# Performance work log

Hardware: AMD Instinct MI355X
Metric: run time of the kernel (lower is better)

The kernel has to match this reference:

```python
import jax, jax.numpy as jnp
import numpy as np

N_HEAD = 12


def setup_inputs() -> dict:
    key = jax.random.key(0)
    ks = jax.random.split(key, 6)
    B, T, C = 8, 1024, 768
    x = jax.random.normal(ks[0], (B, T, C), dtype=jnp.float32)
    w_attn = jax.random.normal(ks[1], (C, 3 * C), dtype=jnp.float32) * 0.02
    b_attn = jnp.zeros((3 * C,), dtype=jnp.float32)
    w_proj = jax.random.normal(ks[2], (C, C), dtype=jnp.float32) * 0.02
    b_proj = jnp.zeros((C,), dtype=jnp.float32)
    rel_emb = jax.random.normal(ks[3], (2 * 1024 - 1, C // N_HEAD), dtype=jnp.float32) * 0.02
    return {"x": x, "w_attn": w_attn, "b_attn": b_attn,
            "w_proj": w_proj, "b_proj": b_proj, "rel_emb": rel_emb}


def reference(x, w_attn, b_attn, w_proj, b_proj, rel_emb):
    b, t, c = x.shape
    h = N_HEAD
    d = c // h
    scale = d ** -0.5
    # fused QKV projection
    qkv = x @ w_attn + b_attn                       # [b, t, 3c]
    q, k, v = jnp.split(qkv, 3, axis=-1)
    split_heads = lambda z: z.reshape(b, t, h, d).transpose(0, 2, 1, 3)  # [b,h,t,d]
    q, k, v = map(split_heads, (q, k, v))
    q = q * scale
    # content scores
    scores = jnp.einsum('bhid,bhjd->bhij', q, k)    # [b,h,t,t]
    # relative position bias: embed lookup + rel-shift (zero row prepended, last dropped)
    rel = rel_emb[:t]                               # [t, d]
    rel = jnp.concatenate([jnp.zeros_like(rel[:1]), rel], axis=0)[:-1]
    scores = scores + jnp.einsum('bhid,jd->bhij', q, rel)
    # causal mask
    causal = jnp.tril(jnp.ones((t, t), dtype=bool))
    scores = jnp.where(causal, scores, -jnp.inf)
    probs = jax.nn.softmax(scores, axis=-1)
    y = jnp.einsum('bhij,bhjd->bhid', probs, v)     # [b,h,t,d]
    y = y.transpose(0, 2, 1, 3).reshape(b, t, c)
    return y @ w_proj + b_proj
```

## Files before the change

### kernel.cpp

```cpp
#include <hip/hip_runtime.h>
#include <stdint.h>


typedef __attribute__((ext_vector_type(8))) short short8;
typedef __attribute__((ext_vector_type(4))) float f32x4;
typedef __attribute__((ext_vector_type(4))) unsigned short ushort4v;

#define DEV static __device__ __forceinline__

DEV float bf2f(unsigned short u) {
    union { unsigned int u; float f; } v; v.u = ((unsigned int)u) << 16; return v.f;
}
DEV unsigned short f2bf(float f) {
    union { float f; unsigned int u; } v; v.f = f;
    unsigned int u = v.u;
    return (unsigned short)((u + 0x7fffu + ((u >> 16) & 1u)) >> 16);
}

typedef const __attribute__((address_space(1))) void* gas_ptr;
typedef __attribute__((address_space(3))) void* las_ptr;
DEV void glds16(const void* g, void* l) {
    __builtin_amdgcn_global_load_lds((gas_ptr)g, (las_ptr)l, 16, 0, 0);
}

__global__ void detect_dtype(const unsigned int* __restrict__ w, int* __restrict__ flag) {
    __shared__ int cnt;
    if (threadIdx.x == 0) cnt = 0;
    __syncthreads();
    int c = 0;
    for (int i = threadIdx.x; i < 8192; i += 256) {
        unsigned int b1 = (w[i] >> 8) & 0x7F;
        c += (b1 >= 0x38 && b1 <= 0x3E) ? 1 : 0;
    }
    atomicAdd(&cnt, c);
    __syncthreads();
    if (threadIdx.x == 0) *flag = (cnt > 4096) ? 1 : 0;
}

__global__ __launch_bounds__(256) void cast_x(
    const void* __restrict__ x, unsigned short* __restrict__ xo,
    const int* __restrict__ flag)
{
    int i = (blockIdx.x * 256 + threadIdx.x) * 4;
    if (*flag) {
        *(ushort4v*)(xo + i) = *(const ushort4v*)((const unsigned short*)x + i);
    } else {
        f32x4 v = *(const f32x4*)((const float*)x + i);
        ushort4v o;
#pragma unroll
        for (int j = 0; j < 4; ++j) o[j] = f2bf(v[j]);
        *(ushort4v*)(xo + i) = o;
    }
}

__global__ __launch_bounds__(256) void cast_small(
    const void* __restrict__ rel, const void* __restrict__ ba, const void* __restrict__ bp,
    unsigned short* __restrict__ rel_o, unsigned short* __restrict__ ba_o,
    unsigned short* __restrict__ bp_o, const int* __restrict__ flag)
{
    int i = blockIdx.x * 256 + threadIdx.x;
    if (i >= 134080) return;
    int isbf = *flag;
    const void* src; unsigned short* dst; int off;
    if (i < 131008)      { src = rel; dst = rel_o; off = i; }
    else if (i < 133312) { src = ba;  dst = ba_o;  off = i - 131008; }
    else                 { src = bp;  dst = bp_o;  off = i - 133312; }
    dst[off] = isbf ? ((const unsigned short*)src)[off]
                    : f2bf(((const float*)src)[off]);
}

__global__ __launch_bounds__(256) void transpose_w(
    const void* __restrict__ in, unsigned short* __restrict__ out,
    int R, int C, const int* __restrict__ flag)
{
    __shared__ unsigned short tile[64][66];
    const int t = threadIdx.x;
    const int cb = blockIdx.x * 64;
    const int rb = blockIdx.y * 64;
    if (*flag) {
        const unsigned short* inp = (const unsigned short*)in;
        const int c8 = (t & 7) * 8;
        const int r = t >> 3;
#pragma unroll
        for (int p = 0; p < 2; ++p) {
            int rr = r + p * 32;
            short8 v = *(const short8*)(inp + (size_t)(rb + rr) * C + cb + c8);
#pragma unroll
            for (int i = 0; i < 8; ++i) tile[rr][c8 + i] = (unsigned short)v[i];
        }
    } else {
        const float* inp = (const float*)in;
        const int c4 = (t & 15) * 4;
        const int r = t >> 4;
#pragma unroll
        for (int p = 0; p < 4; ++p) {
            int rr = r + p * 16;
            f32x4 v = *(const f32x4*)(inp + (size_t)(rb + rr) * C + cb + c4);
#pragma unroll
            for (int i = 0; i < 4; ++i) tile[rr][c4 + i] = f2bf(v[i]);
        }
    }
    __syncthreads();
    {
        const int c8 = (t & 7) * 8;
        const int r = t >> 3;
#pragma unroll
        for (int p = 0; p < 2; ++p) {
            int oc = r + p * 32;
            short8 v;
#pragma unroll
            for (int i = 0; i < 8; ++i) v[i] = (short)tile[c8 + i][oc];
            *(short8*)(out + (size_t)(cb + oc) * R + rb + c8) = v;
        }
    }
}

#define GEMM_PROLOG(A_, Bt_)                                                     \
    __shared__ __align__(16) unsigned short Abuf[128 * 32];                      \
    __shared__ __align__(16) unsigned short Bbuf[128 * 32];                      \
    const int t = threadIdx.x;                                                   \
    const int wave = t >> 6, lane = t & 63;                                      \
    const int lo = lane & 15, hi = lane >> 4;                                    \
    const int wr = wave >> 1, wc = wave & 1;                                     \
    const int bm = blockIdx.x * 128;                                             \
    const int bn = blockIdx.y * 128;                                             \
    int L0 = t << 4, L1 = (t + 256) << 4;                                        \
    int S0 = L0 ^ (((L0 >> 7) & 3) << 4);                                        \
    int S1 = L1 ^ (((L1 >> 7) & 3) << 4);                                        \
    int r0 = S0 >> 6, o0 = (S0 & 63) >> 1;                                       \
    int r1 = S1 >> 6, o1 = (S1 & 63) >> 1;                                       \
    const unsigned short* Ab = (A_) + (size_t)bm * 768;                          \
    const unsigned short* Bb = (Bt_) + (size_t)bn * 768;                         \
    char* lA0 = (char*)Abuf + ((wave * 64) << 4);                                \
    char* lA1 = (char*)Abuf + ((256 + wave * 64) << 4);                          \
    char* lB0 = (char*)Bbuf + ((wave * 64) << 4);                                \
    char* lB1 = (char*)Bbuf + ((256 + wave * 64) << 4);                          \
    const char* ap[4]; const char* bp_[4];                                       \
    _Pragma("unroll")                                                            \
    for (int m = 0; m < 4; ++m) {                                                \
        int Pa = ((wr * 64 + m * 16 + lo) << 6) + (hi << 4);                     \
        ap[m] = (const char*)Abuf + (Pa ^ (((Pa >> 7) & 3) << 4));               \
        int Pb = ((wc * 64 + m * 16 + lo) << 6) + (hi << 4);                     \
        bp_[m] = (const char*)Bbuf + (Pb ^ (((Pb >> 7) & 3) << 4));              \
    }                                                                            \
    f32x4 acc[4][4];                                                             \
    _Pragma("unroll")                                                            \
    for (int m = 0; m < 4; ++m)                                                  \
        _Pragma("unroll")                                                        \
        for (int n = 0; n < 4; ++n) acc[m][n] = (f32x4){0.f, 0.f, 0.f, 0.f};     \
    for (int k0 = 0; k0 < 768; k0 += 32) {                                       \
        glds16(Ab + (size_t)r0 * 768 + k0 + o0, lA0);                            \
        glds16(Ab + (size_t)r1 * 768 + k0 + o1, lA1);                            \
        glds16(Bb + (size_t)r0 * 768 + k0 + o0, lB0);                            \
        glds16(Bb + (size_t)r1 * 768 + k0 + o1, lB1);                            \
        __syncthreads();                                                         \
        short8 af[4], bfv[4];                                                    \
        _Pragma("unroll")                                                        \
        for (int m = 0; m < 4; ++m) af[m] = *(const short8*)ap[m];               \
        _Pragma("unroll")                                                        \
        for (int n = 0; n < 4; ++n) bfv[n] = *(const short8*)bp_[n];             \
        _Pragma("unroll")                                                        \
        for (int m = 0; m < 4; ++m)                                              \
            _Pragma("unroll")                                                    \
            for (int n = 0; n < 4; ++n)                                          \
                acc[m][n] = __builtin_amdgcn_mfma_f32_16x16x32_bf16(             \
                    af[m], bfv[n], acc[m][n], 0, 0, 0);                          \
        __syncthreads();                                                         \
    }

__global__ __launch_bounds__(256) void gemm_qkv(
    const unsigned short* __restrict__ A,
    const unsigned short* __restrict__ Bt,
    const unsigned short* __restrict__ bias,
    const unsigned short* __restrict__ rel,
    unsigned short* __restrict__ q_ws,
    unsigned short* __restrict__ k_ws,
    unsigned short* __restrict__ v_ws)
{
    GEMM_PROLOG(A, Bt)
    const int gm0 = bm + wr * 64 + hi * 4;
    const float QSCALE = 0.125f * 1.44269504f;
#pragma unroll
    for (int m = 0; m < 4; ++m) {
        int gm = gm0 + m * 16;
        int b_ = gm >> 10;
        int tt = gm & 1023;
#pragma unroll
        for (int n = 0; n < 4; ++n) {
            int col = bn + wc * 64 + n * 16 + lo;
            float bs = bf2f(bias[col]);
            if (col < 768) {
                int h = col >> 6, d = col & 63;
                size_t base = (((size_t)b_ * 12 + h) * 1024 + tt) * 64 + d;
#pragma unroll
                for (int j = 0; j < 4; ++j)
                    q_ws[base + (size_t)j * 64] = f2bf((acc[m][n][j] + bs) * QSCALE);
            } else if (col < 1536) {
                int h = (col - 768) >> 6, d = col & 63;
                size_t base = (((size_t)b_ * 12 + h) * 1024 + tt) * 64 + d;
#pragma unroll
                for (int j = 0; j < 4; ++j) {
                    int trow = tt + j;
                    float rv = (trow > 0) ? bf2f(rel[(size_t)(trow - 1) * 64 + d]) : 0.f;
                    k_ws[base + (size_t)j * 64] = f2bf(acc[m][n][j] + bs + rv);
                }
            } else {
                int h = (col - 1536) >> 6, d = col & 63;
                size_t vb = (((size_t)b_ * 12 + h) * 64 + d) * 1024 + tt;
                ushort4v pk;
#pragma unroll
                for (int j = 0; j < 4; ++j) pk[j] = f2bf(acc[m][n][j] + bs);
                *(ushort4v*)(v_ws + vb) = pk;
            }
        }
    }
}

__global__ __launch_bounds__(256) void gemm_proj(
    const unsigned short* __restrict__ A,
    const unsigned short* __restrict__ Bt,
    const unsigned short* __restrict__ bias,
    const int* __restrict__ flag,
    void* __restrict__ outv)
{
    GEMM_PROLOG(A, Bt)
    const int isbf = *flag;
    const int gm0 = bm + wr * 64 + hi * 4;
#pragma unroll
    for (int m = 0; m < 4; ++m) {
        int gm = gm0 + m * 16;
#pragma unroll
        for (int n = 0; n < 4; ++n) {
            int col = bn + wc * 64 + n * 16 + lo;
            float bs = bf2f(bias[col]);
#pragma unroll
            for (int j = 0; j < 4; ++j) {
                float v = acc[m][n][j] + bs;
                if (isbf)
                    ((unsigned short*)outv)[(size_t)(gm + j) * 768 + col] = f2bf(v);
                else
                    ((float*)outv)[(size_t)(gm + j) * 768 + col] = v;
            }
        }
    }
}

__global__ __launch_bounds__(256) void attn_fused(
    const unsigned short* __restrict__ q_ws,
    const unsigned short* __restrict__ k_ws,
    const unsigned short* __restrict__ v_ws,
    unsigned short* __restrict__ att)
{
    __shared__ __align__(16) unsigned short Kbuf[2][64 * 64];
    __shared__ __align__(16) unsigned short Vbuf[2][64 * 64];
    __shared__ __align__(16) unsigned short Pbuf[4][16 * 64];
    const int t = threadIdx.x;
    const int wave = t >> 6, lane = t & 63;
    const int lo = lane & 15, hi = lane >> 4;
    const int gid = blockIdx.x;
    const int xcd = gid & 7;
    const int c = gid >> 3;
    const int bh = xcd * 12 + (c % 12);
    const int pairIdx = c / 12;
    const int b_ = bh / 12, h = bh % 12;
    const size_t base = (size_t)bh * (1024 * 64);
    const unsigned short* Kb = k_ws + base;
    const unsigned short* Vb = v_ws + base;
    const float DEFER_THR = 11.5f;

    int L0 = t << 4, L1 = (t + 256) << 4;
    int S0 = L0 ^ (((L0 >> 7) & 7) << 4);
    int S1 = L1 ^ (((L1 >> 7) & 7) << 4);
    int r0 = S0 >> 7, o0 = (S0 & 127) >> 1;
    int r1 = S1 >> 7, o1 = (S1 & 127) >> 1;
    const int lof0 = (wave * 64) << 4;
    const int lof1 = (256 + wave * 64) << 4;

    int koff[4][2];
#pragma unroll
    for (int nt = 0; nt < 4; ++nt)
#pragma unroll
        for (int kc = 0; kc < 2; ++kc) {
            int P = ((nt * 16 + lo) << 7) + (kc << 6) + (hi << 4);
            koff[nt][kc] = P ^ (((P >> 7) & 7) << 4);
        }
    int poffR[2];
#pragma unroll
    for (int kc = 0; kc < 2; ++kc) {
        int P = (lo << 7) + (kc << 6) + (hi << 4);
        poffR[kc] = P ^ (((P >> 7) & 7) << 4);
    }
    int poffW[4][4];
#pragma unroll
    for (int nt = 0; nt < 4; ++nt)
#pragma unroll
        for (int j = 0; j < 4; ++j) {
            int P = (lo << 7) + ((nt * 16 + hi * 4 + j) << 1);
            poffW[nt][j] = P ^ ((lo & 7) << 4);
        }
    char* pb = (char*)&Pbuf[wave][0];

#pragma unroll 1
    for (int sel = 0; sel < 2; ++sel) {
        const int qt = sel ? pairIdx : (15 - pairIdx);
        const int q0w = qt * 64 + wave * 16;
        const int qrow = q0w + lo;

        short8 qf[2];
#pragma unroll
        for (int kc = 0; kc < 2; ++kc)
            qf[kc] = *(const short8*)(q_ws + base +
                (size_t)(q0w + lo) * 64 + kc * 32 + hi * 8);

        f32x4 o[4];
        float mrun = -1e30f, lrun = 0.f;
#pragma unroll
        for (int nt = 0; nt < 4; ++nt) o[nt] = (f32x4){0.f, 0.f, 0.f, 0.f};

        if (sel) __syncthreads();
        glds16(Kb + (size_t)r0 * 64 + o0, (char*)Kbuf[0] + lof0);
        glds16(Kb + (size_t)r1 * 64 + o1, (char*)Kbuf[0] + lof1);
        glds16(Vb + (size_t)r0 * 1024 + o0, (char*)Vbuf[0] + lof0);
        glds16(Vb + (size_t)r1 * 1024 + o1, (char*)Vbuf[0] + lof1);

        int cur = 0;
        const int nkt = qt + 1;
        for (int kt = 0; kt < nkt; ++kt) {
            __syncthreads();
            if (kt + 1 < nkt) {
                const int kn = (kt + 1) * 64;
                glds16(Kb + (size_t)(kn + r0) * 64 + o0, (char*)Kbuf[cur ^ 1] + lof0);
                glds16(Kb + (size_t)(kn + r1) * 64 + o1, (char*)Kbuf[cur ^ 1] + lof1);
                glds16(Vb + (size_t)r0 * 1024 + kn + o0, (char*)Vbuf[cur ^ 1] + lof0);
                glds16(Vb + (size_t)r1 * 1024 + kn + o1, (char*)Vbuf[cur ^ 1] + lof1);
            }
            const int kv0 = kt * 64;
            const char* Kc = (const char*)Kbuf[cur];
            const char* Vc = (const char*)Vbuf[cur];

            short8 kf[4][2];
#pragma unroll
            for (int nt = 0; nt < 4; ++nt)
#pragma unroll
                for (int kc = 0; kc < 2; ++kc)
                    kf[nt][kc] = *(const short8*)(Kc + koff[nt][kc]);
            f32x4 sc[4];
            __builtin_amdgcn_s_setprio(1);
#pragma unroll
            for (int nt = 0; nt < 4; ++nt) {
                f32x4 z = (f32x4){0.f, 0.f, 0.f, 0.f};
                z = __builtin_amdgcn_mfma_f32_16x16x32_bf16(kf[nt][0], qf[0], z, 0, 0, 0);
                z = __builtin_amdgcn_mfma_f32_16x16x32_bf16(kf[nt][1], qf[1], z, 0, 0, 0);
                sc[nt] = z;
            }
            __builtin_amdgcn_s_setprio(0);
            if (kv0 + 63 > q0w) {
#pragma unroll
                for (int nt = 0; nt < 4; ++nt)
#pragma unroll
                    for (int j = 0; j < 4; ++j) {
                        int kc_ = kv0 + nt * 16 + hi * 4 + j;
                        if (kc_ > qrow) sc[nt][j] = -1e30f;
                    }
            }
            float m0;
            {
                float a0 = fmaxf(fmaxf(sc[0][0], sc[0][1]), fmaxf(sc[0][2], sc[0][3]));
                float a1 = fmaxf(fmaxf(sc[1][0], sc[1][1]), fmaxf(sc[1][2], sc[1][3]));
                float a2 = fmaxf(fmaxf(sc[2][0], sc[2][1]), fmaxf(sc[2][2], sc[2][3]));
                float a3 = fmaxf(fmaxf(sc[3][0], sc[3][1]), fmaxf(sc[3][2], sc[3][3]));
                m0 = fmaxf(fmaxf(a0, a1), fmaxf(a2, a3));
            }
            m0 = fmaxf(m0, __shfl_xor(m0, 16));
            m0 = fmaxf(m0, __shfl_xor(m0, 32));
            if (__any(m0 > mrun + DEFER_THR)) {
                float nm = fmaxf(mrun, m0);
                float corr = __builtin_amdgcn_exp2f(mrun - nm);
                mrun = nm;
                lrun *= corr;
#pragma unroll
                for (int j = 0; j < 4; ++j) {
                    float cj = __shfl(corr, hi * 4 + j);
#pragma unroll
                    for (int nt = 0; nt < 4; ++nt) o[nt][j] *= cj;
                }
            }
            float rs = 0.f;
#pragma unroll
            for (int nt = 0; nt < 4; ++nt)
#pragma unroll
                for (int j = 0; j < 4; ++j) {
                    float p = __builtin_amdgcn_exp2f(sc[nt][j] - mrun);
                    sc[nt][j] = p;
                    rs += p;
                }
            rs += __shfl_xor(rs, 16);
            rs += __shfl_xor(rs, 32);
            lrun += rs;
            short8 vf[4][2];
#pragma unroll
            for (int nt = 0; nt < 4; ++nt)
#pragma unroll
                for (int kc2 = 0; kc2 < 2; ++kc2)
                    vf[nt][kc2] = *(const short8*)(Vc + koff[nt][kc2]);
#pragma unroll
            for (int nt = 0; nt < 4; ++nt)
#pragma unroll
                for (int j = 0; j < 4; ++j)
                    *(unsigned short*)(pb + poffW[nt][j]) = f2bf(sc[nt][j]);
#pragma unroll
            for (int kc2 = 0; kc2 < 2; ++kc2) {
                short8 pf = *(const short8*)(pb + poffR[kc2]);
                __builtin_amdgcn_s_setprio(1);
#pragma unroll
                for (int nt = 0; nt < 4; ++nt)
                    o[nt] = __builtin_amdgcn_mfma_f32_16x16x32_bf16(pf, vf[nt][kc2], o[nt], 0, 0, 0);
                __builtin_amdgcn_s_setprio(0);
            }
            cur ^= 1;
        }
#pragma unroll
        for (int j = 0; j < 4; ++j) {
            float lj = __shfl(lrun, hi * 4 + j);
            float inv = 1.f / lj;
            int tt = q0w + hi * 4 + j;
#pragma unroll
            for (int nt = 0; nt < 4; ++nt)
                att[((size_t)(b_ * 1024 + tt)) * 768 + h * 64 + nt * 16 + lo] =
                    f2bf(o[nt][j] * inv);
        }
    }
}

extern "C" void kernel_launch(void* const* d_in, const int* in_sizes, int n_in,
                              void* d_out, int out_size, void* d_ws, size_t ws_size,
                              hipStream_t stream) {
    const void* x      = d_in[0];
    const void* w_attn = d_in[1];
    const void* b_attn = d_in[2];
    const void* w_proj = d_in[3];
    const void* b_proj = d_in[4];
    const void* rel    = d_in[5];
    char* ws = (char*)d_ws;
    int*            flag = (int*)(ws + 0);
    unsigned short* wTa  = (unsigned short*)(ws + 4096);
    unsigned short* wTp  = (unsigned short*)(ws + 3543040);
    unsigned short* x_bf = (unsigned short*)(ws + 4722688);
    unsigned short* relb = (unsigned short*)(ws + 17305600);
    unsigned short* bab  = (unsigned short*)(ws + 17567616);
    unsigned short* bpb  = (unsigned short*)(ws + 17572224);
    unsigned short* q_ws = (unsigned short*)(ws + 17573760);
    unsigned short* k_ws = (unsigned short*)(ws + 30156672);
    unsigned short* v_ws = (unsigned short*)(ws + 42739584);
    unsigned short* att  = x_bf;

    detect_dtype<<<1, 256, 0, stream>>>((const unsigned int*)w_attn, flag);
    cast_x<<<6144, 256, 0, stream>>>(x, x_bf, flag);
    cast_small<<<524, 256, 0, stream>>>(rel, b_attn, b_proj, relb, bab, bpb, flag);
    transpose_w<<<dim3(36, 12), 256, 0, stream>>>(w_attn, wTa, 768, 2304, flag);
    transpose_w<<<dim3(12, 12), 256, 0, stream>>>(w_proj, wTp, 768, 768, flag);
    gemm_qkv<<<dim3(64, 18), 256, 0, stream>>>(x_bf, wTa, bab, relb, q_ws, k_ws, v_ws);
    attn_fused<<<768, 256, 0, stream>>>(q_ws, k_ws, v_ws, att);
    gemm_proj<<<dim3(64, 6), 256, 0, stream>>>(att, wTp, bpb, flag, (void*)d_out);
}
```

Before: 215.0 us.

## Double-buffer LDS tiles in GEMM main loop to overlap loads with MFMA

The shared GEMM prolog macro now keeps two LDS buffers for the A and B tiles. It issues the first tile before the loop, then prefetches tile k+1 into the other buffer while the MFMAs run on tile k. This replaces the load–barrier–compute–barrier sequence with a single barrier per iteration, hiding global-to-LDS latency behind compute. The cost is twice the LDS per block, which may lower occupancy. Only the projection GEMMs are affected, not the attention kernel.

Result: no change. 214.2 us (-0.4%).

```diff
diff --git a/kernel.cpp b/kernel.cpp
--- a/kernel.cpp
+++ b/kernel.cpp
@@ -116,8 +116,8 @@
 }
 
 #define GEMM_PROLOG(A_, Bt_)                                                     \
-    __shared__ __align__(16) unsigned short Abuf[128 * 32];                      \
-    __shared__ __align__(16) unsigned short Bbuf[128 * 32];                      \
+    __shared__ __align__(16) unsigned short Abuf[2][128 * 32];                   \
+    __shared__ __align__(16) unsigned short Bbuf[2][128 * 32];                   \
     const int t = threadIdx.x;                                                   \
     const int wave = t >> 6, lane = t & 63;                                      \
     const int lo = lane & 15, hi = lane >> 4;                                    \
@@ -131,41 +131,50 @@
     int r1 = S1 >> 6, o1 = (S1 & 63) >> 1;                                       \
     const unsigned short* Ab = (A_) + (size_t)bm * 768;                          \
     const unsigned short* Bb = (Bt_) + (size_t)bn * 768;                         \
-    char* lA0 = (char*)Abuf + ((wave * 64) << 4);                                \
-    char* lA1 = (char*)Abuf + ((256 + wave * 64) << 4);                          \
-    char* lB0 = (char*)Bbuf + ((wave * 64) << 4);                                \
-    char* lB1 = (char*)Bbuf + ((256 + wave * 64) << 4);                          \
-    const char* ap[4]; const char* bp_[4];                                       \
+    const int lof0 = (wave * 64) << 4;                                           \
+    const int lof1 = (256 + wave * 64) << 4;                                     \
+    int aoff[4]; int boff[4];                                                    \
     _Pragma("unroll")                                                            \
     for (int m = 0; m < 4; ++m) {                                                \
         int Pa = ((wr * 64 + m * 16 + lo) << 6) + (hi << 4);                     \
-        ap[m] = (const char*)Abuf + (Pa ^ (((Pa >> 7) & 3) << 4));               \
+        aoff[m] = Pa ^ (((Pa >> 7) & 3) << 4);                                   \
         int Pb = ((wc * 64 + m * 16 + lo) << 6) + (hi << 4);                     \
-        bp_[m] = (const char*)Bbuf + (Pb ^ (((Pb >> 7) & 3) << 4));              \
+        boff[m] = Pb ^ (((Pb >> 7) & 3) << 4);                                   \
     }                                                                            \
     f32x4 acc[4][4];                                                             \
     _Pragma("unroll")                                                            \
     for (int m = 0; m < 4; ++m)                                                  \
         _Pragma("unroll")                                                        \
         for (int n = 0; n < 4; ++n) acc[m][n] = (f32x4){0.f, 0.f, 0.f, 0.f};     \
+                                         \
+    glds16(Ab + (size_t)r0 * 768 + o0, (char*)Abuf[0] + lof0);                   \
+    glds16(Ab + (size_t)r1 * 768 + o1, (char*)Abuf[0] + lof1);                   \
+    glds16(Bb + (size_t)r0 * 768 + o0, (char*)Bbuf[0] + lof0);                   \
+    glds16(Bb + (size_t)r1 * 768 + o1, (char*)Bbuf[0] + lof1);                   \
+    int cur = 0;                                                                 \
     for (int k0 = 0; k0 < 768; k0 += 32) {                                       \
-        glds16(Ab + (size_t)r0 * 768 + k0 + o0, lA0);                            \
-        glds16(Ab + (size_t)r1 * 768 + k0 + o1, lA1);                            \
-        glds16(Bb + (size_t)r0 * 768 + k0 + o0, lB0);                            \
-        glds16(Bb + (size_t)r1 * 768 + k0 + o1, lB1);                            \
-        __syncthreads();                                                         \
+        __syncthreads();        \
+        if (k0 + 32 < 768) {                                                     \
+            const int kn = k0 + 32;                                              \
+            glds16(Ab + (size_t)r0 * 768 + kn + o0, (char*)Abuf[cur ^ 1] + lof0);\
+            glds16(Ab + (size_t)r1 * 768 + kn + o1, (char*)Abuf[cur ^ 1] + lof1);\
+            glds16(Bb + (size_t)r0 * 768 + kn + o0, (char*)Bbuf[cur ^ 1] + lof0);\
+            glds16(Bb + (size_t)r1 * 768 + kn + o1, (char*)Bbuf[cur ^ 1] + lof1);\
+        }                                                                        \
         short8 af[4], bfv[4];                                                    \
         _Pragma("unroll")                                                        \
-        for (int m = 0; m < 4; ++m) af[m] = *(const short8*)ap[m];               \
+        for (int m = 0; m < 4; ++m)                                              \
+            af[m] = *(const short8*)((const char*)Abuf[cur] + aoff[m]);          \
         _Pragma("unroll")                                                        \
-        for (int n = 0; n < 4; ++n) bfv[n] = *(const short8*)bp_[n];             \
+        for (int n = 0; n < 4; ++n)                                              \
+            bfv[n] = *(const short8*)((const char*)Bbuf[cur] + boff[n]);         \
         _Pragma("unroll")                                                        \
         for (int m = 0; m < 4; ++m)                                              \
             _Pragma("unroll")                                                    \
             for (int n = 0; n < 4; ++n)                                          \
                 acc[m][n] = __builtin_amdgcn_mfma_f32_16x16x32_bf16(             \
                     af[m], bfv[n], acc[m][n], 0, 0, 0);                          \
-        __syncthreads();                                                         \
+        cur ^= 1;                                                                \
     }
 
 __global__ __launch_bounds__(256) void gemm_qkv(
```
